# Performance work log

Hardware: AMD Instinct MI355X
Metric: run time of the kernel (lower is better)

The kernel has to match this reference:

```python
import jax, jax.numpy as jnp
import numpy as np

EPS = 1e-6
NUM_HEADS = 8
NUM_TOKENS = 196

def setup_inputs() -> dict:
    key = jax.random.key(0)
    ks = jax.random.split(key, 4)
    B, N, C = 32, 3136, 384
    H, Dh, M = NUM_HEADS, C // NUM_HEADS, NUM_TOKENS
    return {
        "x": jax.random.normal(ks[0], (B, N, C), dtype=jnp.float32),
        "q_param": jax.random.normal(ks[1], (1, M, H, Dh), dtype=jnp.float32) * 0.02,
        "kv_w": jax.random.normal(ks[2], (2 * C, C), dtype=jnp.float32) * 0.02,
        "proj_w": jax.random.normal(ks[3], (C, C), dtype=jnp.float32) * 0.02,
        "proj_b": jnp.zeros((C,), dtype=jnp.float32),
        "ln_w": jnp.ones((C,), dtype=jnp.float32),
        "ln_b": jnp.zeros((C,), dtype=jnp.float32),
    }

def reference(x, q_param, kv_w, proj_w, proj_b, ln_w, ln_b):
    B, N, C = x.shape
    H = NUM_HEADS
    Dh = C // H
    # LayerNorm (eps=1e-6)
    mu = jnp.mean(x, axis=-1, keepdims=True)
    var = jnp.mean(jnp.square(x - mu), axis=-1, keepdims=True)
    x = (x - mu) * jax.lax.rsqrt(var + EPS) * ln_w + ln_b
    # exact GELU (nn.GELU default)
    x = jax.nn.gelu(x, approximate=False)
    # kv projection (no bias): [B,N,2C] -> k,v each [B,H,N,Dh]
    kv = (x @ kv_w.T).reshape(B, N, 2, H, Dh)
    kv = jnp.transpose(kv, (2, 0, 3, 1, 4))
    k, v = kv[0], kv[1]
    # learnable queries: (1,M,H,Dh) -> (1,H,M,Dh)
    q = jnp.transpose(q_param, (0, 2, 1, 3))
    # NOTE: source applies NO 1/sqrt(Dh) scaling
    attn = jnp.einsum("bhmd,bhnd->bhmn", jnp.broadcast_to(q, (B, H, NUM_TOKENS, Dh)), k)
    attn = jax.nn.softmax(attn, axis=-1)
    out = jnp.einsum("bhmn,bhnd->bhmd", attn, v)  # [B,H,M,Dh]
    out = jnp.transpose(out, (0, 2, 1, 3)).reshape(B, NUM_TOKENS, C)
    return out @ proj_w.T + proj_b
```

## Files before the change

kernel.cpp:

```cpp
#include <hip/hip_runtime.h>
#include <stdint.h>

typedef float f32x4 __attribute__((ext_vector_type(4)));
typedef short s16x8 __attribute__((ext_vector_type(8)));
typedef short s16x4 __attribute__((ext_vector_type(4)));
typedef unsigned short ushort_t;

#define B_  32
#define N_  3136
#define C_  384
#define H_  8
#define DH_ 48
#define M_  196
#define ROWS  (B_*N_)
#define PROWS (B_*M_)

static __device__ __forceinline__ ushort_t f2bf(float f) {
  union { float f; uint32_t u; } v; v.f = f;
  uint32_t r = (v.u + 0x7fffu + ((v.u >> 16) & 1u)) >> 16;
  return (ushort_t)r;
}
static __device__ __forceinline__ ushort_t f2bf_fast(float f) {
  union { float f; uint32_t u; } v; v.f = f;
  return (ushort_t)((v.u + 0x8000u) >> 16);
}

static __device__ __forceinline__ f32x4 mfma_16x16x32(s16x8 a, s16x8 b, f32x4 c) {
  return __builtin_amdgcn_mfma_f32_16x16x32_bf16(a, b, c, 0, 0, 0);
}

static __device__ __forceinline__ f32x4 mfma_16x16x16(s16x4 a, s16x4 b, f32x4 c) {
#if __has_builtin(__builtin_amdgcn_mfma_f32_16x16x16_bf16)
  return __builtin_amdgcn_mfma_f32_16x16x16_bf16(a, b, c, 0, 0, 0);
#elif __has_builtin(__builtin_amdgcn_mfma_f32_16x16x16bf16_1k)
  return __builtin_amdgcn_mfma_f32_16x16x16bf16_1k(a, b, c, 0, 0, 0);
#else
  f32x4 d;
  asm("v_mfma_f32_16x16x16_bf16 %0, %1, %2, %3" : "=v"(d) : "v"(a), "v"(b), "v"(c));
  return d;
#endif
}

static __device__ __forceinline__ void gload_lds16(const void* g, void* l) {
  __builtin_amdgcn_global_load_lds(
      (const __attribute__((address_space(1))) void*)(uintptr_t)g,
      (__attribute__((address_space(3))) void*)(uint32_t)(uintptr_t)l,
      16, 0, 0);
}

__global__ __launch_bounds__(256) void k_ln_gelu(
    const float* __restrict__ x, const float* __restrict__ lnw,
    const float* __restrict__ lnb, ushort_t* __restrict__ x16) {
  int row = blockIdx.x * 4 + (threadIdx.x >> 6);
  int lane = threadIdx.x & 63;
  const float2* xr = (const float2*)(x + (size_t)row * C_);
  float2 v0 = xr[lane], v1 = xr[lane + 64], v2 = xr[lane + 128];
  float s  = v0.x + v0.y + v1.x + v1.y + v2.x + v2.y;
  float ss = v0.x*v0.x + v0.y*v0.y + v1.x*v1.x + v1.y*v1.y + v2.x*v2.x + v2.y*v2.y;
#pragma unroll
  for (int off = 1; off < 64; off <<= 1) {
    s  += __shfl_xor(s, off);
    ss += __shfl_xor(ss, off);
  }
  float mu = s * (1.0f / C_);
  float rs = rsqrtf(ss * (1.0f / C_) - mu * mu + 1e-6f);
  const float2* wr = (const float2*)lnw;
  const float2* br = (const float2*)lnb;
  uint32_t* outp = (uint32_t*)(x16 + (size_t)row * C_);
#pragma unroll
  for (int t = 0; t < 3; ++t) {
    int idx = lane + t * 64;
    float2 v = (t == 0) ? v0 : ((t == 1) ? v1 : v2);
    float2 w = wr[idx], bb = br[idx];
    float a0 = (v.x - mu) * rs * w.x + bb.x;
    float a1 = (v.y - mu) * rs * w.y + bb.y;
    a0 = 0.5f * a0 * (1.0f + erff(a0 * 0.70710678118654752440f));
    a1 = 0.5f * a1 * (1.0f + erff(a1 * 0.70710678118654752440f));
    outp[idx] = (uint32_t)f2bf_fast(a0) | ((uint32_t)f2bf_fast(a1) << 16);
  }
}

__global__ __launch_bounds__(256) void k_convert(
    const float* __restrict__ kvw, const float* __restrict__ pw,
    const float* __restrict__ qp, ushort_t* __restrict__ wkv16,
    ushort_t* __restrict__ wp16, ushort_t* __restrict__ q16) {
  int i = blockIdx.x * 256 + threadIdx.x;
  if (i < 2 * C_ * C_) wkv16[i] = f2bf(kvw[i]);
  if (i < C_ * C_)     wp16[i]  = f2bf(pw[i]);
  if (i < M_ * H_ * DH_) {
    int d = i % DH_; int t = i / DH_; int h = t % H_; int m = t / H_;
    q16[((size_t)h * M_ + m) * DH_ + d] = f2bf(qp[i]);
  }
}

template <typename OutT, bool BIAS, bool SWZ>
__global__ __launch_bounds__(256) void k_gemm_bt(
    const ushort_t* __restrict__ A, const ushort_t* __restrict__ Bw,
    OutT* __restrict__ Co, const float* __restrict__ bias,
    int M, int N, int K, int ntn) {
  __shared__ ushort_t lA[2][128 * 32];
  __shared__ ushort_t lB[2][128 * 32];
  int bid = blockIdx.x;
  if (SWZ) bid = (bid & 7) * (gridDim.x >> 3) + (bid >> 3);
  int tr = bid / ntn, tc = bid % ntn;
  int tid = threadIdx.x;
  int w = tid >> 6, l = tid & 63;
  int wr = w >> 1, wc = w & 1;
  int c = l & 15, g = l >> 4;
  f32x4 acc[4][4];
#pragma unroll
  for (int i = 0; i < 4; ++i)
#pragma unroll
    for (int j = 0; j < 4; ++j) acc[i][j] = (f32x4){0.f, 0.f, 0.f, 0.f};
  const size_t a0 = (size_t)tr * 128, b0 = (size_t)tc * 128;
  int srow = l >> 2;
  int scol = (l & 3) * 8;
#pragma unroll
  for (int r = 0; r < 2; ++r) {
    int lr = w * 16 + r * 64;
    gload_lds16(A  + (a0 + lr + srow) * (size_t)K + scol, &lA[0][lr * 32]);
    gload_lds16(Bw + (b0 + lr + srow) * (size_t)K + scol, &lB[0][lr * 32]);
  }
  __syncthreads();
  const int T = K >> 5;
  for (int t = 0; t < T; ++t) {
    int cur = t & 1;
    if (t + 1 < T) {
      int kt = (t + 1) << 5;
#pragma unroll
      for (int r = 0; r < 2; ++r) {
        int lr = w * 16 + r * 64;
        gload_lds16(A  + (a0 + lr + srow) * (size_t)K + kt + scol, &lA[cur ^ 1][lr * 32]);
        gload_lds16(Bw + (b0 + lr + srow) * (size_t)K + kt + scol, &lB[cur ^ 1][lr * 32]);
      }
    }
    s16x8 af[4], bf[4];
#pragma unroll
    for (int i = 0; i < 4; ++i)
      af[i] = *(const s16x8*)&lA[cur][(wr * 64 + i * 16 + c) * 32 + g * 8];
#pragma unroll
    for (int j = 0; j < 4; ++j)
      bf[j] = *(const s16x8*)&lB[cur][(wc * 64 + j * 16 + c) * 32 + g * 8];
#pragma unroll
    for (int i = 0; i < 4; ++i)
#pragma unroll
      for (int j = 0; j < 4; ++j)
        acc[i][j] = mfma_16x16x32(af[i], bf[j], acc[i][j]);
    __syncthreads();
  }
#pragma unroll
  for (int i = 0; i < 4; ++i) {
#pragma unroll
    for (int j = 0; j < 4; ++j) {
      size_t col = b0 + wc * 64 + j * 16 + c;
      float bs = BIAS ? bias[col] : 0.0f;
#pragma unroll
      for (int q = 0; q < 4; ++q) {
        size_t row = a0 + wr * 64 + i * 16 + g * 4 + q;
        float v = acc[i][j][q] + bs;
        if constexpr (sizeof(OutT) == 2) Co[row * N + col] = f2bf(v);
        else                             Co[row * N + col] = v;
      }
    }
  }
}

__global__ __launch_bounds__(512) void k_attn(
    const ushort_t* __restrict__ kv, const ushort_t* __restrict__ q16,
    ushort_t* __restrict__ att16) {
  int b = blockIdx.x >> 3, h = blockIdx.x & 7;
  __shared__ ushort_t Kl[64 * 72];
  __shared__ ushort_t Vt[48 * 76];
  int tid = threadIdx.x;
  int w = tid >> 6, l = tid & 63;
  int c = l & 15, g = l >> 4;
  for (int i = tid; i < 64 * 72; i += 512) Kl[i] = 0;
  for (int i = tid; i < 48 * 76; i += 512) Vt[i] = 0;
  s16x8 qf[2][2];
#pragma unroll
  for (int i = 0; i < 2; ++i)
#pragma unroll
    for (int kk = 0; kk < 2; ++kk) {
      int m = w * 32 + i * 16 + c;
      int dh = kk * 32 + g * 8;
      s16x8 z = {0, 0, 0, 0, 0, 0, 0, 0};
      qf[i][kk] = (m < M_ && dh < DH_)
                      ? *(const s16x8*)(q16 + ((size_t)h * M_ + m) * DH_ + dh)
                      : z;
    }
  f32x4 o[3][2];
#pragma unroll
  for (int f = 0; f < 3; ++f)
#pragma unroll
    for (int i = 0; i < 2; ++i) o[f][i] = (f32x4){0.f, 0.f, 0.f, 0.f};
  float rm[2] = {-3e38f, -3e38f}, rl[2] = {0.f, 0.f};
  int srow = tid >> 3, spart = tid & 7;
  const size_t rowstride = (size_t)(2 * C_);
  uint32_t kr0, kr1, kr2, vr0, vr1, vr2;
  {
    size_t gb = ((size_t)b * N_ + srow) * rowstride + h * DH_ + spart * 6;
    kr0 = *(const uint32_t*)(kv + gb);
    kr1 = *(const uint32_t*)(kv + gb + 2);
    kr2 = *(const uint32_t*)(kv + gb + 4);
    vr0 = *(const uint32_t*)(kv + gb + C_);
    vr1 = *(const uint32_t*)(kv + gb + C_ + 2);
    vr2 = *(const uint32_t*)(kv + gb + C_ + 4);
  }
  __syncthreads();

  for (int t = 0; t < 49; ++t) {
    uint32_t* kd = (uint32_t*)&Kl[srow * 72 + spart * 6];
    kd[0] = kr0; kd[1] = kr1; kd[2] = kr2;
    int dbase = spart * 6;
    Vt[(dbase + 0) * 76 + srow] = (ushort_t)vr0;
    Vt[(dbase + 1) * 76 + srow] = (ushort_t)(vr0 >> 16);
    Vt[(dbase + 2) * 76 + srow] = (ushort_t)vr1;
    Vt[(dbase + 3) * 76 + srow] = (ushort_t)(vr1 >> 16);
    Vt[(dbase + 4) * 76 + srow] = (ushort_t)vr2;
    Vt[(dbase + 5) * 76 + srow] = (ushort_t)(vr2 >> 16);
    __syncthreads();
    {
      int tn = (t < 48) ? t + 1 : t;
      size_t gb = ((size_t)b * N_ + tn * 64 + srow) * rowstride + h * DH_ + spart * 6;
      kr0 = *(const uint32_t*)(kv + gb);
      kr1 = *(const uint32_t*)(kv + gb + 2);
      kr2 = *(const uint32_t*)(kv + gb + 4);
      vr0 = *(const uint32_t*)(kv + gb + C_);
      vr1 = *(const uint32_t*)(kv + gb + C_ + 2);
      vr2 = *(const uint32_t*)(kv + gb + C_ + 4);
    }
    f32x4 s[4][2];
#pragma unroll
    for (int j = 0; j < 4; ++j) {
      s16x8 kf0 = *(const s16x8*)&Kl[(j * 16 + c) * 72 + g * 8];
      s16x8 kf1 = *(const s16x8*)&Kl[(j * 16 + c) * 72 + 32 + g * 8];
#pragma unroll
      for (int i = 0; i < 2; ++i) {
        f32x4 z = {0.f, 0.f, 0.f, 0.f};
        f32x4 t0 = mfma_16x16x32(kf0, qf[i][0], z);
        s[j][i] = mfma_16x16x32(kf1, qf[i][1], t0);
      }
    }
    s16x4 pb[2][4];
#pragma unroll
    for (int i = 0; i < 2; ++i) {
      float tm = s[0][i][0];
#pragma unroll
      for (int j = 0; j < 4; ++j)
#pragma unroll
        for (int q = 0; q < 4; ++q) tm = fmaxf(tm, s[j][i][q]);
      tm = fmaxf(tm, __shfl_xor(tm, 16));
      tm = fmaxf(tm, __shfl_xor(tm, 32));
      float nm = fmaxf(rm[i], tm);
      float corr = __expf(rm[i] - nm);
      rm[i] = nm;
      float ts = 0.f;
#pragma unroll
      for (int j = 0; j < 4; ++j) {
        float p0 = __expf(s[j][i][0] - nm);
        float p1 = __expf(s[j][i][1] - nm);
        float p2 = __expf(s[j][i][2] - nm);
        float p3 = __expf(s[j][i][3] - nm);
        ts += (p0 + p1) + (p2 + p3);
        pb[i][j] = (s16x4){(short)f2bf_fast(p0), (short)f2bf_fast(p1),
                           (short)f2bf_fast(p2), (short)f2bf_fast(p3)};
      }
      ts += __shfl_xor(ts, 16);
      ts += __shfl_xor(ts, 32);
      rl[i] = rl[i] * corr + ts;
#pragma unroll
      for (int f = 0; f < 3; ++f) o[f][i] *= corr;
    }
#pragma unroll
    for (int f = 0; f < 3; ++f)
#pragma unroll
      for (int j = 0; j < 4; ++j) {
        s16x4 vf = *(const s16x4*)&Vt[(f * 16 + c) * 76 + j * 16 + g * 4];
        o[f][0] = mfma_16x16x16(vf, pb[0][j], o[f][0]);
        o[f][1] = mfma_16x16x16(vf, pb[1][j], o[f][1]);
      }
    __syncthreads();
  }
#pragma unroll
  for (int i = 0; i < 2; ++i) {
    int m = w * 32 + i * 16 + c;
    if (m < M_) {
      float inv = 1.0f / rl[i];
#pragma unroll
      for (int f = 0; f < 3; ++f) {
        uint32_t w0 = (uint32_t)f2bf_fast(o[f][i][0] * inv) |
                      ((uint32_t)f2bf_fast(o[f][i][1] * inv) << 16);
        uint32_t w1 = (uint32_t)f2bf_fast(o[f][i][2] * inv) |
                      ((uint32_t)f2bf_fast(o[f][i][3] * inv) << 16);
        uint2 val; val.x = w0; val.y = w1;
        *(uint2*)&att16[((size_t)b * M_ + m) * C_ + h * DH_ + f * 16 + g * 4] = val;
      }
    }
  }
}

extern "C" void kernel_launch(void* const* d_in, const int* in_sizes, int n_in,
                              void* d_out, int out_size, void* d_ws, size_t ws_size,
                              hipStream_t stream) {
  (void)in_sizes; (void)n_in; (void)out_size; (void)ws_size;
  const float* x   = (const float*)d_in[0];
  const float* qp  = (const float*)d_in[1];
  const float* kvw = (const float*)d_in[2];
  const float* pw  = (const float*)d_in[3];
  const float* pbv = (const float*)d_in[4];
  const float* lnw = (const float*)d_in[5];
  const float* lnb = (const float*)d_in[6];
  float* out = (float*)d_out;

  ushort_t* x16   = (ushort_t*)d_ws;
  ushort_t* kv16  = x16 + (size_t)ROWS * C_;
  ushort_t* att16 = kv16 + (size_t)ROWS * 2 * C_;
  ushort_t* wkv16 = att16 + (size_t)PROWS * C_;
  ushort_t* wp16  = wkv16 + 2 * C_ * C_;
  ushort_t* q16   = wp16 + C_ * C_;

  hipLaunchKernelGGL(k_ln_gelu, dim3(ROWS / 4), dim3(256), 0, stream, x, lnw, lnb, x16);
  hipLaunchKernelGGL(k_convert, dim3((2 * C_ * C_ + 255) / 256), dim3(256), 0, stream,
                     kvw, pw, qp, wkv16, wp16, q16);
  hipLaunchKernelGGL((k_gemm_bt<ushort_t, false, true>),
                     dim3((ROWS / 128) * (2 * C_ / 128)), dim3(256), 0, stream,
                     x16, wkv16, kv16, (const float*)nullptr, ROWS, 2 * C_, C_, 2 * C_ / 128);
  hipLaunchKernelGGL(k_attn, dim3(B_ * H_), dim3(512), 0, stream, kv16, q16, att16);
  hipLaunchKernelGGL((k_gemm_bt<float, true, false>),
                     dim3((PROWS / 128) * (C_ / 128)), dim3(256), 0, stream,
                     att16, wp16, out, pbv, PROWS, C_, C_, C_ / 128);
}
```

Before: 265.3 us.

## Split attention KV sequence into four chunks with a combine kernel

The attention kernel now runs one block per (batch, head, KV chunk), splitting the 49 key tiles into four chunks. Each block writes an unnormalised partial output plus its running max and sum to a workspace that reuses the x16 buffer. A new combine kernel merges the four partials by rescaling with exp(m - max) and writes the bf16 attention output. The aim is to raise the block count from 256 to 1024 so the GPU is better filled and the serial loop is shorter. The cost is extra fp32 partial traffic and one more launch. Separately, the GEMM main loop swaps __syncthreads for explicit vmcnt waits plus raw s_barrier, so the next tile's async loads can stay in flight across the barrier.

```diff
diff --git a/kernel.cpp b/kernel.cpp
--- a/kernel.cpp
+++ b/kernel.cpp
@@ -14,6 +14,7 @@
 #define M_  196
 #define ROWS  (B_*N_)
 #define PROWS (B_*M_)
+#define NCHUNK 4
 
 static __device__ __forceinline__ ushort_t f2bf(float f) {
   union { float f; uint32_t u; } v; v.f = f;
@@ -121,7 +122,6 @@
     gload_lds16(A  + (a0 + lr + srow) * (size_t)K + scol, &lA[0][lr * 32]);
     gload_lds16(Bw + (b0 + lr + srow) * (size_t)K + scol, &lB[0][lr * 32]);
   }
-  __syncthreads();
   const int T = K >> 5;
   for (int t = 0; t < T; ++t) {
     int cur = t & 1;
@@ -133,7 +133,12 @@
         gload_lds16(A  + (a0 + lr + srow) * (size_t)K + kt + scol, &lA[cur ^ 1][lr * 32]);
         gload_lds16(Bw + (b0 + lr + srow) * (size_t)K + kt + scol, &lB[cur ^ 1][lr * 32]);
       }
-    }
+      asm volatile("s_waitcnt vmcnt(4)" ::: "memory");
+    } else {
+      asm volatile("s_waitcnt vmcnt(0)" ::: "memory");
+    }
+    __builtin_amdgcn_sched_barrier(0);
+    __builtin_amdgcn_s_barrier();
     s16x8 af[4], bf[4];
 #pragma unroll
     for (int i = 0; i < 4; ++i)
@@ -146,7 +151,8 @@
 #pragma unroll
       for (int j = 0; j < 4; ++j)
         acc[i][j] = mfma_16x16x32(af[i], bf[j], acc[i][j]);
-    __syncthreads();
+    __builtin_amdgcn_sched_barrier(0);
+    __builtin_amdgcn_s_barrier();
   }
 #pragma unroll
   for (int i = 0; i < 4; ++i) {
@@ -167,8 +173,12 @@
 
 __global__ __launch_bounds__(512) void k_attn(
     const ushort_t* __restrict__ kv, const ushort_t* __restrict__ q16,
-    ushort_t* __restrict__ att16) {
-  int b = blockIdx.x >> 3, h = blockIdx.x & 7;
+    float* __restrict__ Opart, float2* __restrict__ mlp) {
+  int slot = blockIdx.x;
+  int chunk = slot & (NCHUNK - 1), bh = slot >> 2;
+  int b = bh >> 3, h = bh & 7;
+  int tile0 = (chunk == 0) ? 0 : (12 * chunk + 1);
+  int tile1 = tile0 + ((chunk == 0) ? 13 : 12);
   __shared__ ushort_t Kl[64 * 72];
   __shared__ ushort_t Vt[48 * 76];
   int tid = threadIdx.x;
@@ -198,7 +208,7 @@
   const size_t rowstride = (size_t)(2 * C_);
   uint32_t kr0, kr1, kr2, vr0, vr1, vr2;
   {
-    size_t gb = ((size_t)b * N_ + srow) * rowstride + h * DH_ + spart * 6;
+    size_t gb = ((size_t)b * N_ + tile0 * 64 + srow) * rowstride + h * DH_ + spart * 6;
     kr0 = *(const uint32_t*)(kv + gb);
     kr1 = *(const uint32_t*)(kv + gb + 2);
     kr2 = *(const uint32_t*)(kv + gb + 4);
@@ -208,7 +218,7 @@
   }
   __syncthreads();
 
-  for (int t = 0; t < 49; ++t) {
+  for (int t = tile0; t < tile1; ++t) {
     uint32_t* kd = (uint32_t*)&Kl[srow * 72 + spart * 6];
     kd[0] = kr0; kd[1] = kr1; kd[2] = kr2;
     int dbase = spart * 6;
@@ -220,7 +230,7 @@
     Vt[(dbase + 5) * 76 + srow] = (ushort_t)(vr2 >> 16);
     __syncthreads();
     {
-      int tn = (t < 48) ? t + 1 : t;
+      int tn = (t < tile1 - 1) ? t + 1 : t;
       size_t gb = ((size_t)b * N_ + tn * 64 + srow) * rowstride + h * DH_ + spart * 6;
       kr0 = *(const uint32_t*)(kv + gb);
       kr1 = *(const uint32_t*)(kv + gb + 2);
@@ -285,17 +295,43 @@
   for (int i = 0; i < 2; ++i) {
     int m = w * 32 + i * 16 + c;
     if (m < M_) {
-      float inv = 1.0f / rl[i];
-#pragma unroll
-      for (int f = 0; f < 3; ++f) {
-        uint32_t w0 = (uint32_t)f2bf_fast(o[f][i][0] * inv) |
-                      ((uint32_t)f2bf_fast(o[f][i][1] * inv) << 16);
-        uint32_t w1 = (uint32_t)f2bf_fast(o[f][i][2] * inv) |
-                      ((uint32_t)f2bf_fast(o[f][i][3] * inv) << 16);
-        uint2 val; val.x = w0; val.y = w1;
-        *(uint2*)&att16[((size_t)b * M_ + m) * C_ + h * DH_ + f * 16 + g * 4] = val;
-      }
-    }
+#pragma unroll
+      for (int f = 0; f < 3; ++f)
+        *(f32x4*)&Opart[((size_t)slot * M_ + m) * 48 + f * 16 + g * 4] = o[f][i];
+      if (g == 0) {
+        float2 v; v.x = rm[i]; v.y = rl[i];
+        mlp[slot * M_ + m] = v;
+      }
+    }
+  }
+}
+
+__global__ __launch_bounds__(256) void k_combine(
+    const float* __restrict__ Opart, const float2* __restrict__ mlp,
+    ushort_t* __restrict__ att16) {
+  int wid = blockIdx.x * 4 + (threadIdx.x >> 6);
+  int lane = threadIdx.x & 63;
+  int bh = wid / M_, m = wid - bh * M_;
+  int b = bh >> 3, h = bh & 7;
+  float mc[NCHUNK], lc[NCHUNK];
+#pragma unroll
+  for (int cc = 0; cc < NCHUNK; ++cc) {
+    float2 v = mlp[(bh * NCHUNK + cc) * M_ + m];
+    mc[cc] = v.x; lc[cc] = v.y;
+  }
+  float Mx = fmaxf(fmaxf(mc[0], mc[1]), fmaxf(mc[2], mc[3]));
+  float L = 0.f, sc[NCHUNK];
+#pragma unroll
+  for (int cc = 0; cc < NCHUNK; ++cc) {
+    sc[cc] = __expf(mc[cc] - Mx);
+    L += sc[cc] * lc[cc];
+  }
+  if (lane < 48) {
+    float od = 0.f;
+#pragma unroll
+    for (int cc = 0; cc < NCHUNK; ++cc)
+      od += sc[cc] * Opart[((size_t)(bh * NCHUNK + cc) * M_ + m) * 48 + lane];
+    att16[((size_t)b * M_ + m) * C_ + h * DH_ + lane] = f2bf_fast(od / L);
   }
 }
 
@@ -318,6 +354,8 @@
   ushort_t* wkv16 = att16 + (size_t)PROWS * C_;
   ushort_t* wp16  = wkv16 + 2 * C_ * C_;
   ushort_t* q16   = wp16 + C_ * C_;
+  float*  Opart = (float*)d_ws;
+  float2* mlp   = (float2*)(Opart + (size_t)(B_ * H_ * NCHUNK) * M_ * 48);
 
   hipLaunchKernelGGL(k_ln_gelu, dim3(ROWS / 4), dim3(256), 0, stream, x, lnw, lnb, x16);
   hipLaunchKernelGGL(k_convert, dim3((2 * C_ * C_ + 255) / 256), dim3(256), 0, stream,
@@ -325,7 +363,10 @@
   hipLaunchKernelGGL((k_gemm_bt<ushort_t, false, true>),
                      dim3((ROWS / 128) * (2 * C_ / 128)), dim3(256), 0, stream,
                      x16, wkv16, kv16, (const float*)nullptr, ROWS, 2 * C_, C_, 2 * C_ / 128);
-  hipLaunchKernelGGL(k_attn, dim3(B_ * H_), dim3(512), 0, stream, kv16, q16, att16);
+  hipLaunchKernelGGL(k_attn, dim3(B_ * H_ * NCHUNK), dim3(512), 0, stream,
+                     kv16, q16, Opart, mlp);
+  hipLaunchKernelGGL(k_combine, dim3(B_ * H_ * M_ / 4), dim3(256), 0, stream,
+                     Opart, mlp, att16);
   hipLaunchKernelGGL((k_gemm_bt<float, true, false>),
                      dim3((PROWS / 128) * (C_ / 128)), dim3(256), 0, stream,
                      att16, wp16, out, pbv, PROWS, C_, C_, C_ / 128);
```

Result: slower. 272.0 us (+2.5%).

## Triple-buffer GEMM LDS with swizzle; split attention query rows across blocks

Applied to the files above, without the earlier changes.

The GEMM now uses a three-stage LDS ring with explicit vmcnt waits and raw barriers, plus an XOR swizzle on LDS columns to reduce bank conflicts on fragment reads. The attention kernel splits the 196 query rows across two 256-thread blocks per (batch, head). It double-buffers the K/V LDS tiles, which removes one barrier per iteration, and uses wider 8-byte global loads. This raises grid parallelism and overlap, at the cost of each K/V tile being loaded twice (once per half) and more LDS per block.

```diff
diff --git a/kernel.cpp b/kernel.cpp
--- a/kernel.cpp
+++ b/kernel.cpp
@@ -98,8 +98,8 @@
     const ushort_t* __restrict__ A, const ushort_t* __restrict__ Bw,
     OutT* __restrict__ Co, const float* __restrict__ bias,
     int M, int N, int K, int ntn) {
-  __shared__ ushort_t lA[2][128 * 32];
-  __shared__ ushort_t lB[2][128 * 32];
+  __shared__ ushort_t lA[3][128 * 32];
+  __shared__ ushort_t lB[3][128 * 32];
   int bid = blockIdx.x;
   if (SWZ) bid = (bid & 7) * (gridDim.x >> 3) + (bid >> 3);
   int tr = bid / ntn, tc = bid % ntn;
@@ -114,39 +114,61 @@
     for (int j = 0; j < 4; ++j) acc[i][j] = (f32x4){0.f, 0.f, 0.f, 0.f};
   const size_t a0 = (size_t)tr * 128, b0 = (size_t)tc * 128;
   int srow = l >> 2;
-  int scol = (l & 3) * 8;
+  int scol = (((l & 3) ^ ((l >> 3) & 3))) * 8;
+  const int rsw = (c >> 1) & 3;
+  const int T = K >> 5;
 #pragma unroll
   for (int r = 0; r < 2; ++r) {
     int lr = w * 16 + r * 64;
     gload_lds16(A  + (a0 + lr + srow) * (size_t)K + scol, &lA[0][lr * 32]);
     gload_lds16(Bw + (b0 + lr + srow) * (size_t)K + scol, &lB[0][lr * 32]);
   }
-  __syncthreads();
-  const int T = K >> 5;
+  if (T > 1) {
+#pragma unroll
+    for (int r = 0; r < 2; ++r) {
+      int lr = w * 16 + r * 64;
+      gload_lds16(A  + (a0 + lr + srow) * (size_t)K + 32 + scol, &lA[1][lr * 32]);
+      gload_lds16(Bw + (b0 + lr + srow) * (size_t)K + 32 + scol, &lB[1][lr * 32]);
+    }
+  }
+  int cur = 0, nxt2 = 2;
   for (int t = 0; t < T; ++t) {
-    int cur = t & 1;
-    if (t + 1 < T) {
-      int kt = (t + 1) << 5;
+    if (t + 2 < T) {
+      int kt = (t + 2) << 5;
 #pragma unroll
       for (int r = 0; r < 2; ++r) {
         int lr = w * 16 + r * 64;
-        gload_lds16(A  + (a0 + lr + srow) * (size_t)K + kt + scol, &lA[cur ^ 1][lr * 32]);
-        gload_lds16(Bw + (b0 + lr + srow) * (size_t)K + kt + scol, &lB[cur ^ 1][lr * 32]);
-      }
-    }
+        gload_lds16(A  + (a0 + lr + srow) * (size_t)K + kt + scol, &lA[nxt2][lr * 32]);
+        gload_lds16(Bw + (b0 + lr + srow) * (size_t)K + kt + scol, &lB[nxt2][lr * 32]);
+      }
+      asm volatile("s_waitcnt vmcnt(8)" ::: "memory");
+    } else if (t + 1 < T) {
+      asm volatile("s_waitcnt vmcnt(4)" ::: "memory");
+    } else {
+      asm volatile("s_waitcnt vmcnt(0)" ::: "memory");
+    }
+    __builtin_amdgcn_sched_barrier(0);
+    __builtin_amdgcn_s_barrier();
     s16x8 af[4], bf[4];
 #pragma unroll
-    for (int i = 0; i < 4; ++i)
-      af[i] = *(const s16x8*)&lA[cur][(wr * 64 + i * 16 + c) * 32 + g * 8];
-#pragma unroll
-    for (int j = 0; j < 4; ++j)
-      bf[j] = *(const s16x8*)&lB[cur][(wc * 64 + j * 16 + c) * 32 + g * 8];
+    for (int i = 0; i < 4; ++i) {
+      int row = wr * 64 + i * 16 + c;
+      af[i] = *(const s16x8*)&lA[cur][row * 32 + ((unsigned)(g ^ rsw)) * 8];
+    }
+#pragma unroll
+    for (int j = 0; j < 4; ++j) {
+      int row = wc * 64 + j * 16 + c;
+      bf[j] = *(const s16x8*)&lB[cur][row * 32 + ((unsigned)(g ^ rsw)) * 8];
+    }
 #pragma unroll
     for (int i = 0; i < 4; ++i)
 #pragma unroll
       for (int j = 0; j < 4; ++j)
         acc[i][j] = mfma_16x16x32(af[i], bf[j], acc[i][j]);
-    __syncthreads();
+    __builtin_amdgcn_sched_barrier(0);
+    __builtin_amdgcn_s_barrier();
+    cur = (cur == 2) ? 0 : cur + 1;
+    nxt2 = (nxt2 == 2) ? 0 : nxt2 + 1;
   }
 #pragma unroll
   for (int i = 0; i < 4; ++i) {
@@ -165,23 +187,23 @@
   }
 }
 
-__global__ __launch_bounds__(512) void k_attn(
+__global__ __launch_bounds__(256) void k_attn(
     const ushort_t* __restrict__ kv, const ushort_t* __restrict__ q16,
     ushort_t* __restrict__ att16) {
-  int b = blockIdx.x >> 3, h = blockIdx.x & 7;
-  __shared__ ushort_t Kl[64 * 72];
-  __shared__ ushort_t Vt[48 * 76];
+  int bh = blockIdx.x >> 1, half = blockIdx.x & 1;
+  int b = bh >> 3, h = bh & 7;
+  __shared__ ushort_t Kl[2][64 * 72];
+  __shared__ ushort_t Vt[2][48 * 76];
   int tid = threadIdx.x;
   int w = tid >> 6, l = tid & 63;
   int c = l & 15, g = l >> 4;
-  for (int i = tid; i < 64 * 72; i += 512) Kl[i] = 0;
-  for (int i = tid; i < 48 * 76; i += 512) Vt[i] = 0;
+  for (int i = tid; i < 2 * 64 * 72; i += 256) ((ushort_t*)Kl)[i] = 0;
   s16x8 qf[2][2];
 #pragma unroll
   for (int i = 0; i < 2; ++i)
 #pragma unroll
     for (int kk = 0; kk < 2; ++kk) {
-      int m = w * 32 + i * 16 + c;
+      int m = half * 128 + w * 32 + i * 16 + c;
       int dh = kk * 32 + g * 8;
       s16x8 z = {0, 0, 0, 0, 0, 0, 0, 0};
       qf[i][kk] = (m < M_ && dh < DH_)
@@ -194,46 +216,47 @@
 #pragma unroll
     for (int i = 0; i < 2; ++i) o[f][i] = (f32x4){0.f, 0.f, 0.f, 0.f};
   float rm[2] = {-3e38f, -3e38f}, rl[2] = {0.f, 0.f};
-  int srow = tid >> 3, spart = tid & 7;
+  int srow = tid >> 2, spart = tid & 3;
   const size_t rowstride = (size_t)(2 * C_);
-  uint32_t kr0, kr1, kr2, vr0, vr1, vr2;
+  const size_t gbase = (size_t)b * N_ * rowstride + h * DH_ + spart * 12;
+  uint2 kA, kB, kC, vA, vB, vC;
   {
-    size_t gb = ((size_t)b * N_ + srow) * rowstride + h * DH_ + spart * 6;
-    kr0 = *(const uint32_t*)(kv + gb);
-    kr1 = *(const uint32_t*)(kv + gb + 2);
-    kr2 = *(const uint32_t*)(kv + gb + 4);
-    vr0 = *(const uint32_t*)(kv + gb + C_);
-    vr1 = *(const uint32_t*)(kv + gb + C_ + 2);
-    vr2 = *(const uint32_t*)(kv + gb + C_ + 4);
+    const ushort_t* p = kv + gbase + (size_t)srow * rowstride;
+    kA = *(const uint2*)(p);      kB = *(const uint2*)(p + 4);  kC = *(const uint2*)(p + 8);
+    vA = *(const uint2*)(p + C_); vB = *(const uint2*)(p + C_ + 4); vC = *(const uint2*)(p + C_ + 8);
   }
   __syncthreads();
 
   for (int t = 0; t < 49; ++t) {
-    uint32_t* kd = (uint32_t*)&Kl[srow * 72 + spart * 6];
-    kd[0] = kr0; kd[1] = kr1; kd[2] = kr2;
-    int dbase = spart * 6;
-    Vt[(dbase + 0) * 76 + srow] = (ushort_t)vr0;
-    Vt[(dbase + 1) * 76 + srow] = (ushort_t)(vr0 >> 16);
-    Vt[(dbase + 2) * 76 + srow] = (ushort_t)vr1;
-    Vt[(dbase + 3) * 76 + srow] = (ushort_t)(vr1 >> 16);
-    Vt[(dbase + 4) * 76 + srow] = (ushort_t)vr2;
-    Vt[(dbase + 5) * 76 + srow] = (ushort_t)(vr2 >> 16);
+    int p = t & 1;
+    uint2* kd = (uint2*)&Kl[p][srow * 72 + spart * 12];
+    kd[0] = kA; kd[1] = kB; kd[2] = kC;
+    int dbase = spart * 12;
+    ushort_t* vt = &Vt[p][0];
+    vt[(dbase + 0) * 76 + srow]  = (ushort_t)vA.x;
+    vt[(dbase + 1) * 76 + srow]  = (ushort_t)(vA.x >> 16);
+    vt[(dbase + 2) * 76 + srow]  = (ushort_t)vA.y;
+    vt[(dbase + 3) * 76 + srow]  = (ushort_t)(vA.y >> 16);
+    vt[(dbase + 4) * 76 + srow]  = (ushort_t)vB.x;
+    vt[(dbase + 5) * 76 + srow]  = (ushort_t)(vB.x >> 16);
+    vt[(dbase + 6) * 76 + srow]  = (ushort_t)vB.y;
+    vt[(dbase + 7) * 76 + srow]  = (ushort_t)(vB.y >> 16);
+    vt[(dbase + 8) * 76 + srow]  = (ushort_t)vC.x;
+    vt[(dbase + 9) * 76 + srow]  = (ushort_t)(vC.x >> 16);
+    vt[(dbase + 10) * 76 + srow] = (ushort_t)vC.y;
+    vt[(dbase + 11) * 76 + srow] = (ushort_t)(vC.y >> 16);
     __syncthreads();
     {
       int tn = (t < 48) ? t + 1 : t;
-      size_t gb = ((size_t)b * N_ + tn * 64 + srow) * rowstride + h * DH_ + spart * 6;
-      kr0 = *(const uint32_t*)(kv + gb);
-      kr1 = *(const uint32_t*)(kv + gb + 2);
-      kr2 = *(const uint32_t*)(kv + gb + 4);
-      vr0 = *(const uint32_t*)(kv + gb + C_);
-      vr1 = *(const uint32_t*)(kv + gb + C_ + 2);
-      vr2 = *(const uint32_t*)(kv + gb + C_ + 4);
+      const ushort_t* pp = kv + gbase + ((size_t)tn * 64 + srow) * rowstride;
+      kA = *(const uint2*)(pp);      kB = *(const uint2*)(pp + 4);  kC = *(const uint2*)(pp + 8);
+      vA = *(const uint2*)(pp + C_); vB = *(const uint2*)(pp + C_ + 4); vC = *(const uint2*)(pp + C_ + 8);
     }
     f32x4 s[4][2];
 #pragma unroll
     for (int j = 0; j < 4; ++j) {
-      s16x8 kf0 = *(const s16x8*)&Kl[(j * 16 + c) * 72 + g * 8];
-      s16x8 kf1 = *(const s16x8*)&Kl[(j * 16 + c) * 72 + 32 + g * 8];
+      s16x8 kf0 = *(const s16x8*)&Kl[p][(j * 16 + c) * 72 + g * 8];
+      s16x8 kf1 = *(const s16x8*)&Kl[p][(j * 16 + c) * 72 + 32 + g * 8];
 #pragma unroll
       for (int i = 0; i < 2; ++i) {
         f32x4 z = {0.f, 0.f, 0.f, 0.f};
@@ -275,15 +298,14 @@
     for (int f = 0; f < 3; ++f)
 #pragma unroll
       for (int j = 0; j < 4; ++j) {
-        s16x4 vf = *(const s16x4*)&Vt[(f * 16 + c) * 76 + j * 16 + g * 4];
+        s16x4 vf = *(const s16x4*)&Vt[p][(f * 16 + c) * 76 + j * 16 + g * 4];
         o[f][0] = mfma_16x16x16(vf, pb[0][j], o[f][0]);
         o[f][1] = mfma_16x16x16(vf, pb[1][j], o[f][1]);
       }
-    __syncthreads();
   }
 #pragma unroll
   for (int i = 0; i < 2; ++i) {
-    int m = w * 32 + i * 16 + c;
+    int m = half * 128 + w * 32 + i * 16 + c;
     if (m < M_) {
       float inv = 1.0f / rl[i];
 #pragma unroll
@@ -325,7 +347,7 @@
   hipLaunchKernelGGL((k_gemm_bt<ushort_t, false, true>),
                      dim3((ROWS / 128) * (2 * C_ / 128)), dim3(256), 0, stream,
                      x16, wkv16, kv16, (const float*)nullptr, ROWS, 2 * C_, C_, 2 * C_ / 128);
-  hipLaunchKernelGGL(k_attn, dim3(B_ * H_), dim3(512), 0, stream, kv16, q16, att16);
+  hipLaunchKernelGGL(k_attn, dim3(B_ * H_ * 2), dim3(256), 0, stream, kv16, q16, att16);
   hipLaunchKernelGGL((k_gemm_bt<float, true, false>),
                      dim3((PROWS / 128) * (C_ / 128)), dim3(256), 0, stream,
                      att16, wp16, out, pbv, PROWS, C_, C_, C_ / 128);
```

New measurement: 265.0 us. Within noise of the previous version (-0.1%).
